# Kernel optimization log

Hardware: AMD Instinct MI355X
Metric: run time of the kernel (lower is better)

Reference implementation:

```python
import jax, jax.numpy as jnp
import numpy as np

MEM = 8192
FEAT = 512
B = 16
TAU_NEW = 0.85
D_MIN = 1.5
ALPHA = 0.5
EPS = 1e-8


def setup_inputs() -> dict:
    key = jax.random.key(0)
    k0, k1, k2, k3, k4, k5 = jax.random.split(key, 6)
    adj = (jax.random.uniform(k4, (MEM, MEM)) < 0.001).astype(jnp.float32)
    adj = jnp.maximum(adj, adj.T)  # symmetric, like the original writes
    return {
        "h_t": jax.random.normal(k0, (B, FEAT), jnp.float32),
        "current_position": jax.random.normal(k1, (B, 3), jnp.float32) * 3.0,
        "dones": jnp.zeros((B,), bool),
        "node_features": jax.random.normal(k2, (MEM, FEAT), jnp.float32),
        "node_positions": jax.random.normal(k3, (MEM, 3), jnp.float32) * 3.0,
        "adjacency_matrix": adj,
        "num_nodes": 4096,
        "ptr": 0,
        "last_visited_node_idx": jax.random.randint(k5, (B,), 0, 4096, jnp.int32),
    }


def reference(h_t, current_position, dones, node_features, node_positions,
              adjacency_matrix, num_nodes, ptr, last_visited_node_idx):
    M = node_features.shape[0]
    bsz = h_t.shape[0]
    idxs = jnp.arange(M)
    n0 = jnp.asarray(num_nodes, jnp.int32)
    p0 = jnp.asarray(ptr, jnp.int32)

    def step(state, xs):
        feat, pos, adj, p, n, lastv = state
        h_i, pos_i, done, i = xs
        # masked cosine-similarity search over active nodes (memory-bound matvec)
        fn = jnp.linalg.norm(feat, axis=-1)            # [M]
        hn = jnp.linalg.norm(h_i)
        sims = (feat @ h_i) / (jnp.maximum(fn, EPS) * jnp.maximum(hn, EPS))
        sims = jnp.where(idxs < n, sims, -2.0)
        best = jnp.argmax(sims).astype(jnp.int32)
        max_sim = sims[best]
        dist = jnp.linalg.norm(pos_i - pos[best])

        empty = n < 1
        should_add = (max_sim < TAU_NEW) | (dist > D_MIN)
        has_room = n < M
        # write index per branch: empty->0, add&room->n, add&full->ptr, else EMA at best
        widx = jnp.where(empty, 0,
                         jnp.where(should_add,
                                   jnp.where(has_room, n, p), best)).astype(jnp.int32)
        ema = (~empty) & (~should_add)
        new_f = jnp.where(ema, ALPHA * feat[widx] + (1.0 - ALPHA) * h_i, h_i)
        new_p = jnp.where(ema, ALPHA * pos[widx] + (1.0 - ALPHA) * pos_i, pos_i)
        # done -> no-op write
        new_f = jnp.where(done, feat[widx], new_f)
        new_p = jnp.where(done, pos[widx], new_p)
        feat = feat.at[widx].set(new_f)
        pos = pos.at[widx].set(new_p)
        n2 = n + jnp.where((~done) & (empty | (should_add & has_room)), 1, 0).astype(jnp.int32)
        p2 = jnp.where((~done) & (~empty) & should_add & (~has_room), (p + 1) % M, p)

        cur = widx
        last = lastv[i]
        do_edge = (~done) & (last != -1) & (last != cur)
        lc = jnp.clip(last, 0, M - 1)
        adj = adj.at[lc, cur].set(jnp.where(do_edge, 1.0, adj[lc, cur]))
        adj = adj.at[cur, lc].set(jnp.where(do_edge, 1.0, adj[cur, lc]))
        lastv = lastv.at[i].set(jnp.where(done, -1, cur))
        topo = jnp.where(done, 0.0, adj[cur].sum())
        return (feat, pos, adj, p2, n2, lastv), topo

    xs = (h_t, current_position, dones, jnp.arange(bsz, dtype=jnp.int32))
    state0 = (node_features, node_positions, adjacency_matrix, p0, n0,
              jnp.asarray(last_visited_node_idx, jnp.int32))
    _, topos = jax.lax.scan(step, state0, xs)
    return topos.reshape(bsz, 1)
```

## Files before the change

### kernel.cpp

```cpp
#include <hip/hip_runtime.h>
#include <cfloat>

#define MEMN 8192
#define FEATD 512
#define BATCH 16

static constexpr float TAU_NEW_C = 0.85f;
static constexpr float D_MIN_C  = 1.5f;
static constexpr float ALPHA_C  = 0.5f;
static constexpr float EPS_C    = 1e-8f;


__global__ __launch_bounds__(256) void score_pre_k(
    const float* __restrict__ h_t, const float* __restrict__ feat,
    const float* __restrict__ adj, const int* __restrict__ num_nodes,
    float* __restrict__ pv, int* __restrict__ pi,
    float* __restrict__ pre, float* __restrict__ hn, float* __restrict__ cross) {
  __shared__ float sh[BATCH * FEATD];
  __shared__ float red[256];
  __shared__ float sv[4][BATCH]; __shared__ int si[4][BATCH];
  const int b = blockIdx.x;
  const int tid = threadIdx.x;
  const int wave = tid >> 6, lane = tid & 63;

  if (b < 256) {
    for (int k = tid; k < BATCH * FEATD; k += 256) sh[k] = h_t[k];
    __syncthreads();
    const int n0 = *num_nodes;
    const int base = lane * 8;
    float best[BATCH]; int bidx[BATCH];
    #pragma unroll
    for (int i = 0; i < BATCH; ++i) { best[i] = -FLT_MAX; bidx[i] = 0x7fffffff; }
    for (int j = 0; j < 8; ++j) {
      const int row = b + ((j * 4 + wave) << 8);
      if (row >= n0) continue;
      const float4* fr = (const float4*)(feat + (size_t)row * FEATD);
      const float4 a0 = fr[lane * 2], a1 = fr[lane * 2 + 1];
      float sq = a0.x*a0.x + a0.y*a0.y + a0.z*a0.z + a0.w*a0.w
               + a1.x*a1.x + a1.y*a1.y + a1.z*a1.z + a1.w*a1.w;
      float acc[BATCH];
      #pragma unroll
      for (int i = 0; i < BATCH; ++i) {
        const float4 b0 = *(const float4*)(sh + i * FEATD + base);
        const float4 b1 = *(const float4*)(sh + i * FEATD + base + 4);
        acc[i] = a0.x*b0.x + a0.y*b0.y + a0.z*b0.z + a0.w*b0.w
               + a1.x*b1.x + a1.y*b1.y + a1.z*b1.z + a1.w*b1.w;
      }
      #pragma unroll
      for (int off = 32; off; off >>= 1) {
        sq += __shfl_down(sq, off);
        #pragma unroll
        for (int i = 0; i < BATCH; ++i) acc[i] += __shfl_down(acc[i], off);
      }
      if (lane == 0) {
        const float inv = 1.0f / fmaxf(sqrtf(sq), EPS_C);
        #pragma unroll
        for (int i = 0; i < BATCH; ++i) {
          const float v = acc[i] * inv;
          if (v > best[i]) { best[i] = v; bidx[i] = row; }
        }
      }
    }
    if (lane == 0) {
      #pragma unroll
      for (int i = 0; i < BATCH; ++i) { sv[wave][i] = best[i]; si[wave][i] = bidx[i]; }
    }
    __syncthreads();
    if (tid < BATCH) {
      float v = sv[0][tid]; int ix = si[0][tid];
      #pragma unroll
      for (int w = 1; w < 4; ++w)
        if (sv[w][tid] > v || (sv[w][tid] == v && si[w][tid] < ix)) { v = sv[w][tid]; ix = si[w][tid]; }
      pv[tid * 256 + b] = v; pi[tid * 256 + b] = ix;
    }
  } else if (b < 272) {
    const int bb = b - 256;
    const int n0 = *num_nodes;
    const int row = min(n0 + bb, MEMN - 1);
    const float4* r4 = (const float4*)(adj + (size_t)row * MEMN);
    float s = 0.f;
    for (int k = tid; k < MEMN / 4; k += 256) { const float4 v = r4[k]; s += v.x + v.y + v.z + v.w; }
    red[tid] = s;
    __syncthreads();
    for (int st = 128; st; st >>= 1) { if (tid < st) red[tid] += red[tid + st]; __syncthreads(); }
    if (tid == 0) pre[bb] = red[0];
    __syncthreads();
    const float* h = h_t + bb * FEATD;
    float sq = 0.f;
    for (int k = tid; k < FEATD; k += 256) { const float x = h[k]; sq += x * x; }
    red[tid] = sq;
    __syncthreads();
    for (int st = 128; st; st >>= 1) { if (tid < st) red[tid] += red[tid + st]; __syncthreads(); }
    if (tid == 0) hn[bb] = sqrtf(red[0]);
  } else {
    for (int k = tid; k < BATCH * FEATD; k += 256) sh[k] = h_t[k];
    __syncthreads();
    const int base = lane * 8;
    for (int jt = 0; jt < 4; ++jt) {
      const int j = jt * 4 + wave;
      const float4 a0 = *(const float4*)(sh + j * FEATD + base);
      const float4 a1 = *(const float4*)(sh + j * FEATD + base + 4);
      float sq = a0.x*a0.x + a0.y*a0.y + a0.z*a0.z + a0.w*a0.w
               + a1.x*a1.x + a1.y*a1.y + a1.z*a1.z + a1.w*a1.w;
      float acc[BATCH];
      #pragma unroll
      for (int i = 0; i < BATCH; ++i) {
        const float4 b0 = *(const float4*)(sh + i * FEATD + base);
        const float4 b1 = *(const float4*)(sh + i * FEATD + base + 4);
        acc[i] = a0.x*b0.x + a0.y*b0.y + a0.z*b0.z + a0.w*b0.w
               + a1.x*b1.x + a1.y*b1.y + a1.z*b1.z + a1.w*b1.w;
      }
      #pragma unroll
      for (int off = 32; off; off >>= 1) {
        sq += __shfl_down(sq, off);
        #pragma unroll
        for (int i = 0; i < BATCH; ++i) acc[i] += __shfl_down(acc[i], off);
      }
      if (lane == 0) {
        const float inv = 1.0f / fmaxf(sqrtf(sq), EPS_C);
        #pragma unroll
        for (int i = 0; i < BATCH; ++i) cross[i * 16 + j] = acc[i] * inv;
      }
    }
  }
}

__global__ __launch_bounds__(256) void val_fb_k(
    const float* __restrict__ h_t, const float* __restrict__ posin,
    const unsigned char* __restrict__ dones, const int* __restrict__ lastv,
    const float* __restrict__ feat, const float* __restrict__ posns,
    const float* __restrict__ adj, const int* __restrict__ num_nodes,
    const int* __restrict__ ptr_in, const float* __restrict__ pv,
    const int* __restrict__ pi, const float* __restrict__ pre,
    const float* __restrict__ hn, const float* __restrict__ cross,
    float* __restrict__ out) {
  const int tid = threadIdx.x;
  const int wave = tid >> 6, lane = tid & 63;
  __shared__ float wv[BATCH][4]; __shared__ int wi[BATCH][4];
  __shared__ float s_out[BATCH];
  __shared__ int s_valid;
  const int n0 = *num_nodes;

  float adjval = 1.f;
  int lastp = -1;
  if (tid < BATCH) {
    lastp = lastv[tid];
    if (lastp != -1) {
      const int lc = min(max(lastp, 0), MEMN - 1);
      const int row = min(n0 + tid, MEMN - 1);
      adjval = adj[(size_t)row * MEMN + lc];
    }
  }

  float v[BATCH]; int ix[BATCH];
  #pragma unroll
  for (int s = 0; s < BATCH; ++s) { v[s] = pv[s * 256 + tid]; ix[s] = pi[s * 256 + tid]; }
  #pragma unroll
  for (int s = 0; s < BATCH; ++s) {
    float bv = v[s]; int bi = ix[s];
    #pragma unroll
    for (int off = 32; off; off >>= 1) {
      const float v2 = __shfl_down(bv, off);
      const int   i2 = __shfl_down(bi, off);
      if (v2 > bv || (v2 == bv && i2 < bi)) { bv = v2; bi = i2; }
    }
    if (lane == 0) { wv[s][wave] = bv; wi[s][wave] = bi; }
  }
  __syncthreads();
  int ok = 1;
  if (tid < BATCH) {
    const int s = tid;
    float bv = wv[s][0]; int bi = wi[s][0];
    #pragma unroll
    for (int w = 1; w < 4; ++w)
      if (wv[s][w] > bv || (wv[s][w] == bv && wi[s][w] < bi)) { bv = wv[s][w]; bi = wi[s][w]; }
    for (int j = 0; j < s; ++j) {
      const float cv2 = cross[s * 16 + j];
      if (cv2 > bv) { bv = cv2; bi = n0 + j; }
    }
    if (bi == 0x7fffffff) ok = 0;
    else {
      const float max_sim = bv / fmaxf(hn[s], EPS_C);
      float px, py, pz;
      if (bi >= n0) { const float* pp = posin + (size_t)(bi - n0) * 3; px = pp[0]; py = pp[1]; pz = pp[2]; }
      else          { const float* pp = posns + (size_t)bi * 3;        px = pp[0]; py = pp[1]; pz = pp[2]; }
      const float dx = posin[s * 3 + 0] - px;
      const float dy = posin[s * 3 + 1] - py;
      const float dz = posin[s * 3 + 2] - pz;
      const float dist = sqrtf(dx * dx + dy * dy + dz * dz);
      const bool should_add = (max_sim < TAU_NEW_C) || (dist > D_MIN_C);
      ok = (!dones[s]) && should_add && (lastp == -1 || lastp < n0);
      float o = pre[s];
      if (lastp != -1 && lastp != n0 + s) { if (adjval == 0.f) o += 1.f; }
      s_out[s] = o;
    }
  }
  const unsigned long long m = __ballot(tid < BATCH ? ok : 1);
  if (tid == 0) s_valid = ((~m == 0ull) && (n0 >= 1) && (n0 + BATCH <= MEMN)) ? 1 : 0;
  __syncthreads();
  if (s_valid) { if (tid < BATCH) out[tid] = s_out[tid]; return; }

  __shared__ float mf[16][FEATD];
  __shared__ float mp[16][3];
  __shared__ int   midx[16];
  __shared__ float sh[FEATD];
  __shared__ float rv[256]; __shared__ int ri[256];
  __shared__ int   edges[64][2];
  __shared__ int   s_n, s_p, s_ec, s_mc;
  __shared__ int   s_done, s_widx, s_ema, s_src, s_dst, s_fb;
  __shared__ float s_delta, s_sum;
  if (tid == 0) { s_n = n0; s_p = *ptr_in; s_ec = 0; s_mc = 0; }
  __syncthreads();

  for (int step = 0; step < BATCH; ++step) {
    for (int k = tid; k < FEATD; k += 256) sh[k] = h_t[step * FEATD + k];
    __syncthreads();
    const int n_cur = s_n, mc = s_mc;

    float bv = -FLT_MAX; int bi = 0x7fffffff;
    for (int r = wave; r < n_cur; r += 4) {
      const float* src = feat + (size_t)r * FEATD;
      for (int k = 0; k < 16; ++k)
        if (k < mc && midx[k] == r) src = mf[k];
      float dot = 0.f, sq2 = 0.f;
      for (int e = lane; e < FEATD; e += 64) {
        const float a = src[e], b2 = sh[e];
        dot += a * b2; sq2 += a * a;
      }
      #pragma unroll
      for (int off = 32; off; off >>= 1) {
        dot += __shfl_down(dot, off);
        sq2 += __shfl_down(sq2, off);
      }
      if (lane == 0) {
        const float vv = dot / fmaxf(sqrtf(sq2), EPS_C);
        if (vv > bv) { bv = vv; bi = r; }
      }
    }
    if (lane == 0) { rv[wave] = bv; ri[wave] = bi; }
    __syncthreads();

    if (tid == 0) {
      float fbv = rv[0]; int fbi = ri[0];
      for (int w = 1; w < 4; ++w)
        if (rv[w] > fbv || (rv[w] == fbv && ri[w] < fbi)) { fbv = rv[w]; fbi = ri[w]; }
      const int n = s_n, p = s_p;
      int best; float max_sim;
      if (n < 1) { best = 0; max_sim = -2.0f; }
      else { best = fbi; max_sim = fbv / fmaxf(hn[step], EPS_C); }
      int bsrc = -1;
      for (int k = 0; k < s_mc; ++k) if (midx[k] == best) bsrc = k;
      float pbx, pby, pbz;
      if (bsrc >= 0) { pbx = mp[bsrc][0]; pby = mp[bsrc][1]; pbz = mp[bsrc][2]; }
      else { const float* pb = posns + (size_t)best * 3; pbx = pb[0]; pby = pb[1]; pbz = pb[2]; }
      const float dx = posin[step * 3 + 0] - pbx;
      const float dy = posin[step * 3 + 1] - pby;
      const float dz = posin[step * 3 + 2] - pbz;
      const float dist = sqrtf(dx * dx + dy * dy + dz * dz);
      const int done = dones[step] ? 1 : 0;
      const bool empty = (n < 1);
      const bool should_add = (max_sim < TAU_NEW_C) || (dist > D_MIN_C);
      const bool has_room = (n < MEMN);
      const int widx = empty ? 0 : (should_add ? (has_room ? n : p) : best);
      const bool ema = (!empty) && (!should_add);
      int srcs = -1;
      for (int k = 0; k < s_mc; ++k) if (midx[k] == widx) srcs = k;
      int dsts = srcs;
      if (!done) {
        if (srcs < 0) { dsts = s_mc; midx[dsts] = widx; s_mc = dsts + 1; }
        if (empty || (should_add && has_room)) s_n = n + 1;
        if ((!empty) && should_add && (!has_room)) s_p = (p + 1) % MEMN;
        const int last = lastv[step];
        if (last != -1 && last != widx) {
          const int lc = min(max(last, 0), MEMN - 1);
          const int ec = s_ec;
          edges[ec][0] = lc;   edges[ec][1] = widx;
          edges[ec + 1][0] = widx; edges[ec + 1][1] = lc;
          s_ec = ec + 2;
        }
      }
      s_done = done; s_widx = widx; s_ema = ema ? 1 : 0; s_src = srcs; s_dst = dsts;
      s_delta = 0.f;
      s_fb = 0;
      if (!done) {
        if (widx >= n0 && widx < n0 + BATCH) s_sum = pre[widx - n0];
        else s_fb = 1;
      }
    }
    __syncthreads();

    if (!s_done) {
      const int widx = s_widx;
      float* dstf = mf[s_dst];
      if (s_ema) {
        const float* srcf = (s_src >= 0) ? mf[s_src] : (feat + (size_t)widx * FEATD);
        for (int k = tid; k < FEATD; k += 256)
          dstf[k] = ALPHA_C * srcf[k] + (1.f - ALPHA_C) * sh[k];
      } else {
        for (int k = tid; k < FEATD; k += 256) dstf[k] = sh[k];
      }
      if (tid < 3) {
        const float sp = (s_src >= 0) ? mp[s_src][tid] : posns[(size_t)widx * 3 + tid];
        mp[s_dst][tid] = s_ema ? (ALPHA_C * sp + (1.f - ALPHA_C) * posin[step * 3 + tid])
                               : posin[step * 3 + tid];
      }
      if (tid < s_ec) {
        const int cur = widx;
        if (edges[tid][0] == cur) {
          const int c = edges[tid][1];
          bool dup = false;
          for (int e2 = 0; e2 < tid; ++e2)
            if (edges[e2][0] == cur && edges[e2][1] == c) dup = true;
          if (!dup && adj[(size_t)cur * MEMN + c] == 0.f) atomicAdd(&s_delta, 1.f);
        }
      }
    }
    __syncthreads();

    if (s_fb) {
      const float* row = adj + (size_t)s_widx * MEMN;
      float s = 0.f;
      for (int k = tid; k < MEMN; k += 256) s += row[k];
      rv[tid] = s;
      __syncthreads();
      for (int st = 128; st; st >>= 1) { if (tid < st) rv[tid] += rv[tid + st]; __syncthreads(); }
      if (tid == 0) s_sum = rv[0];
      __syncthreads();
    }
    if (tid == 0) out[step] = s_done ? 0.f : (s_sum + s_delta);
    __syncthreads();
  }
}

extern "C" void kernel_launch(void* const* d_in, const int* in_sizes, int n_in,
                              void* d_out, int out_size, void* d_ws, size_t ws_size,
                              hipStream_t stream) {
  const float*         h_t       = (const float*)d_in[0];
  const float*         cur_pos   = (const float*)d_in[1];
  const unsigned char* dones     = (const unsigned char*)d_in[2];
  const float*         node_feat = (const float*)d_in[3];
  const float*         node_pos  = (const float*)d_in[4];
  const float*         adj       = (const float*)d_in[5];
  const int*           num_nodes = (const int*)d_in[6];
  const int*           ptr_in    = (const int*)d_in[7];
  const int*           lastv     = (const int*)d_in[8];
  float* out = (float*)d_out;

  float* pv    = (float*)d_ws;
  int*   pi    = (int*)(pv + BATCH * 256);
  float* pre   = (float*)(pi + BATCH * 256);
  float* hn    = pre + BATCH;
  float* cross = hn + BATCH;

  score_pre_k<<<273, 256, 0, stream>>>(h_t, node_feat, adj, num_nodes, pv, pi, pre, hn, cross);
  val_fb_k<<<1, 256, 0, stream>>>(h_t, cur_pos, dones, lastv, node_feat, node_pos,
                                  adj, num_nodes, ptr_in, pv, pi, pre, hn, cross, out);
}
```

Before: 30.07 us.

## Fuse scoring and validation kernels with last-block atomic counter handoff

Merges the two kernels into one 256-block launch. The last block to finish, found through an atomicInc counter and thread fences, runs the validation and fallback path, which removes a kernel launch boundary. The query vectors now live in registers instead of shared memory, and the 16 dot-product reductions use a butterfly transpose so each lane ends up holding one query's sum, cutting the shuffle count. The adjacency row sums and the cross-similarity work are spread over the first 80 scoring blocks. The cost is much higher register pressure, and correctness relies on the counter wrapping back to zero on every call.

Result: slower. 43.22 us (+43.8%).

```diff
diff --git a/kernel.cpp b/kernel.cpp
--- a/kernel.cpp
+++ b/kernel.cpp
@@ -10,161 +10,168 @@
 static constexpr float ALPHA_C  = 0.5f;
 static constexpr float EPS_C    = 1e-8f;
 
-
-__global__ __launch_bounds__(256) void score_pre_k(
-    const float* __restrict__ h_t, const float* __restrict__ feat,
-    const float* __restrict__ adj, const int* __restrict__ num_nodes,
-    float* __restrict__ pv, int* __restrict__ pi,
-    float* __restrict__ pre, float* __restrict__ hn, float* __restrict__ cross) {
-  __shared__ float sh[BATCH * FEATD];
-  __shared__ float red[256];
-  __shared__ float sv[4][BATCH]; __shared__ int si[4][BATCH];
-  const int b = blockIdx.x;
-  const int tid = threadIdx.x;
-  const int wave = tid >> 6, lane = tid & 63;
-
-  if (b < 256) {
-    for (int k = tid; k < BATCH * FEATD; k += 256) sh[k] = h_t[k];
-    __syncthreads();
-    const int n0 = *num_nodes;
-    const int base = lane * 8;
-    float best[BATCH]; int bidx[BATCH];
-    #pragma unroll
-    for (int i = 0; i < BATCH; ++i) { best[i] = -FLT_MAX; bidx[i] = 0x7fffffff; }
-    for (int j = 0; j < 8; ++j) {
-      const int row = b + ((j * 4 + wave) << 8);
-      if (row >= n0) continue;
-      const float4* fr = (const float4*)(feat + (size_t)row * FEATD);
-      const float4 a0 = fr[lane * 2], a1 = fr[lane * 2 + 1];
-      float sq = a0.x*a0.x + a0.y*a0.y + a0.z*a0.z + a0.w*a0.w
-               + a1.x*a1.x + a1.y*a1.y + a1.z*a1.z + a1.w*a1.w;
-      float acc[BATCH];
-      #pragma unroll
-      for (int i = 0; i < BATCH; ++i) {
-        const float4 b0 = *(const float4*)(sh + i * FEATD + base);
-        const float4 b1 = *(const float4*)(sh + i * FEATD + base + 4);
-        acc[i] = a0.x*b0.x + a0.y*b0.y + a0.z*b0.z + a0.w*b0.w
-               + a1.x*b1.x + a1.y*b1.y + a1.z*b1.z + a1.w*b1.w;
-      }
-      #pragma unroll
-      for (int off = 32; off; off >>= 1) {
-        sq += __shfl_down(sq, off);
-        #pragma unroll
-        for (int i = 0; i < BATCH; ++i) acc[i] += __shfl_down(acc[i], off);
-      }
-      if (lane == 0) {
-        const float inv = 1.0f / fmaxf(sqrtf(sq), EPS_C);
-        #pragma unroll
-        for (int i = 0; i < BATCH; ++i) {
-          const float v = acc[i] * inv;
-          if (v > best[i]) { best[i] = v; bidx[i] = row; }
-        }
-      }
-    }
-    if (lane == 0) {
-      #pragma unroll
-      for (int i = 0; i < BATCH; ++i) { sv[wave][i] = best[i]; si[wave][i] = bidx[i]; }
-    }
-    __syncthreads();
-    if (tid < BATCH) {
-      float v = sv[0][tid]; int ix = si[0][tid];
-      #pragma unroll
-      for (int w = 1; w < 4; ++w)
-        if (sv[w][tid] > v || (sv[w][tid] == v && si[w][tid] < ix)) { v = sv[w][tid]; ix = si[w][tid]; }
-      pv[tid * 256 + b] = v; pi[tid * 256 + b] = ix;
-    }
-  } else if (b < 272) {
-    const int bb = b - 256;
-    const int n0 = *num_nodes;
-    const int row = min(n0 + bb, MEMN - 1);
-    const float4* r4 = (const float4*)(adj + (size_t)row * MEMN);
-    float s = 0.f;
-    for (int k = tid; k < MEMN / 4; k += 256) { const float4 v = r4[k]; s += v.x + v.y + v.z + v.w; }
-    red[tid] = s;
-    __syncthreads();
-    for (int st = 128; st; st >>= 1) { if (tid < st) red[tid] += red[tid + st]; __syncthreads(); }
-    if (tid == 0) pre[bb] = red[0];
-    __syncthreads();
-    const float* h = h_t + bb * FEATD;
-    float sq = 0.f;
-    for (int k = tid; k < FEATD; k += 256) { const float x = h[k]; sq += x * x; }
-    red[tid] = sq;
-    __syncthreads();
-    for (int st = 128; st; st >>= 1) { if (tid < st) red[tid] += red[tid + st]; __syncthreads(); }
-    if (tid == 0) hn[bb] = sqrtf(red[0]);
-  } else {
-    for (int k = tid; k < BATCH * FEATD; k += 256) sh[k] = h_t[k];
-    __syncthreads();
-    const int base = lane * 8;
-    for (int jt = 0; jt < 4; ++jt) {
-      const int j = jt * 4 + wave;
-      const float4 a0 = *(const float4*)(sh + j * FEATD + base);
-      const float4 a1 = *(const float4*)(sh + j * FEATD + base + 4);
-      float sq = a0.x*a0.x + a0.y*a0.y + a0.z*a0.z + a0.w*a0.w
-               + a1.x*a1.x + a1.y*a1.y + a1.z*a1.z + a1.w*a1.w;
-      float acc[BATCH];
-      #pragma unroll
-      for (int i = 0; i < BATCH; ++i) {
-        const float4 b0 = *(const float4*)(sh + i * FEATD + base);
-        const float4 b1 = *(const float4*)(sh + i * FEATD + base + 4);
-        acc[i] = a0.x*b0.x + a0.y*b0.y + a0.z*b0.z + a0.w*b0.w
-               + a1.x*b1.x + a1.y*b1.y + a1.z*b1.z + a1.w*b1.w;
-      }
-      #pragma unroll
-      for (int off = 32; off; off >>= 1) {
-        sq += __shfl_down(sq, off);
-        #pragma unroll
-        for (int i = 0; i < BATCH; ++i) acc[i] += __shfl_down(acc[i], off);
-      }
-      if (lane == 0) {
-        const float inv = 1.0f / fmaxf(sqrtf(sq), EPS_C);
-        #pragma unroll
-        for (int i = 0; i < BATCH; ++i) cross[i * 16 + j] = acc[i] * inv;
-      }
-    }
-  }
-}
-
-__global__ __launch_bounds__(256) void val_fb_k(
+__device__ __forceinline__ int brev4(int l) {
+  return ((l & 1) << 3) | ((l & 2) << 1) | ((l & 4) >> 1) | ((l & 8) >> 3);
+}
+__device__ __forceinline__ float dot8(const float4& a0, const float4& a1,
+                                      const float4& b0, const float4& b1) {
+  return a0.x*b0.x + a0.y*b0.y + a0.z*b0.z + a0.w*b0.w
+       + a1.x*b1.x + a1.y*b1.y + a1.z*b1.z + a1.w*b1.w;
+}
+
+__device__ __forceinline__ float tree_reduce16(float acc[BATCH], int lane) {
+  #pragma unroll
+  for (int k = 0; k < 8; ++k) {
+    const bool hi = (lane & 1);
+    const float mine = hi ? acc[k + 8] : acc[k];
+    const float send = hi ? acc[k] : acc[k + 8];
+    acc[k] = mine + __shfl_xor(send, 1);
+  }
+  #pragma unroll
+  for (int k = 0; k < 4; ++k) {
+    const bool hi = (lane & 2);
+    const float mine = hi ? acc[k + 4] : acc[k];
+    const float send = hi ? acc[k] : acc[k + 4];
+    acc[k] = mine + __shfl_xor(send, 2);
+  }
+  #pragma unroll
+  for (int k = 0; k < 2; ++k) {
+    const bool hi = (lane & 4);
+    const float mine = hi ? acc[k + 2] : acc[k];
+    const float send = hi ? acc[k] : acc[k + 2];
+    acc[k] = mine + __shfl_xor(send, 4);
+  }
+  {
+    const bool hi = (lane & 8);
+    const float mine = hi ? acc[1] : acc[0];
+    const float send = hi ? acc[0] : acc[1];
+    acc[0] = mine + __shfl_xor(send, 8);
+  }
+  acc[0] += __shfl_xor(acc[0], 16);
+  acc[0] += __shfl_xor(acc[0], 32);
+  return acc[0];
+}
+
+__global__ __launch_bounds__(256, 1) void fused_k(
     const float* __restrict__ h_t, const float* __restrict__ posin,
     const unsigned char* __restrict__ dones, const int* __restrict__ lastv,
     const float* __restrict__ feat, const float* __restrict__ posns,
     const float* __restrict__ adj, const int* __restrict__ num_nodes,
-    const int* __restrict__ ptr_in, const float* __restrict__ pv,
-    const int* __restrict__ pi, const float* __restrict__ pre,
-    const float* __restrict__ hn, const float* __restrict__ cross,
-    float* __restrict__ out) {
+    const int* __restrict__ ptr_in,
+    float* __restrict__ pv, int* __restrict__ pi, float* __restrict__ pre4,
+    float* __restrict__ hnw, float* __restrict__ cross,
+    unsigned* counter, float* __restrict__ out)
+{
+  const int b = blockIdx.x;
   const int tid = threadIdx.x;
   const int wave = tid >> 6, lane = tid & 63;
-  __shared__ float wv[BATCH][4]; __shared__ int wi[BATCH][4];
-  __shared__ float s_out[BATCH];
-  __shared__ int s_valid;
   const int n0 = *num_nodes;
 
-  float adjval = 1.f;
-  int lastp = -1;
+  __shared__ float sv[4][BATCH]; __shared__ int si[4][BATCH];
+  __shared__ float red4[4];
+  __shared__ int s_last;
+
+  float adjval = 1.f; int lastp = -1;
   if (tid < BATCH) {
     lastp = lastv[tid];
     if (lastp != -1) {
       const int lc = min(max(lastp, 0), MEMN - 1);
-      const int row = min(n0 + tid, MEMN - 1);
-      adjval = adj[(size_t)row * MEMN + lc];
-    }
-  }
-
-  float v[BATCH]; int ix[BATCH];
+      adjval = adj[(size_t)min(n0 + tid, MEMN - 1) * MEMN + lc];
+    }
+  }
+
+  float4 hA[BATCH], hB[BATCH];
   #pragma unroll
-  for (int s = 0; s < BATCH; ++s) { v[s] = pv[s * 256 + tid]; ix[s] = pi[s * 256 + tid]; }
-  #pragma unroll
-  for (int s = 0; s < BATCH; ++s) {
-    float bv = v[s]; int bi = ix[s];
-    #pragma unroll
-    for (int off = 32; off; off >>= 1) {
-      const float v2 = __shfl_down(bv, off);
-      const int   i2 = __shfl_down(bi, off);
-      if (v2 > bv || (v2 == bv && i2 < bi)) { bv = v2; bi = i2; }
-    }
-    if (lane == 0) { wv[s][wave] = bv; wi[s][wave] = bi; }
+  for (int i = 0; i < BATCH; ++i) {
+    const float4* hp = (const float4*)(h_t + i * FEATD + lane * 8);
+    hA[i] = hp[0]; hB[i] = hp[1];
+  }
+
+  float bestv = -FLT_MAX; int besti = 0x7fffffff;
+  for (int j = 0; j < 8; ++j) {
+    const int row = b + ((j * 4 + wave) << 8);
+    if (row >= n0) break;
+    const float4* fr = (const float4*)(feat + (size_t)row * FEATD + lane * 8);
+    const float4 a0 = fr[0], a1 = fr[1];
+    float acc[BATCH];
+    #pragma unroll
+    for (int i = 0; i < BATCH; ++i) acc[i] = dot8(a0, a1, hA[i], hB[i]);
+    float sq = dot8(a0, a1, a0, a1);
+    #pragma unroll
+    for (int m = 1; m <= 32; m <<= 1) sq += __shfl_xor(sq, m);
+    const float dtot = tree_reduce16(acc, lane);
+    const float v = dtot / fmaxf(sqrtf(sq), EPS_C);
+    if (v > bestv) { bestv = v; besti = row; }
+  }
+  if (lane < BATCH) { sv[wave][brev4(lane)] = bestv; si[wave][brev4(lane)] = besti; }
+  __syncthreads();
+  if (tid < BATCH) {
+    float v = sv[0][tid]; int ix = si[0][tid];
+    #pragma unroll
+    for (int w = 1; w < 4; ++w)
+      if (sv[w][tid] > v || (sv[w][tid] == v && si[w][tid] < ix)) { v = sv[w][tid]; ix = si[w][tid]; }
+    pv[tid * 256 + b] = v; pi[tid * 256 + b] = ix;
+  }
+
+  if (b < 64) {
+    const int row = min(n0 + (b >> 2), MEMN - 1);
+    const float4* r4 = (const float4*)(adj + (size_t)row * MEMN + (size_t)(b & 3) * 2048);
+    const float4 q0 = r4[tid], q1 = r4[tid + 256];
+    float s = q0.x+q0.y+q0.z+q0.w + q1.x+q1.y+q1.z+q1.w;
+    #pragma unroll
+    for (int m = 1; m <= 32; m <<= 1) s += __shfl_xor(s, m);
+    if (lane == 0) red4[wave] = s;
+    __syncthreads();
+    if (tid == 0) pre4[b] = red4[0] + red4[1] + red4[2] + red4[3];
+  } else if (b < 80) {
+    const int j = b - 64;
+    if (wave == 0) {
+      float4 c0 = hA[0], c1 = hB[0];
+      #pragma unroll
+      for (int jj = 1; jj < BATCH; ++jj) if (j == jj) { c0 = hA[jj]; c1 = hB[jj]; }
+      float acc[BATCH];
+      #pragma unroll
+      for (int i = 0; i < BATCH; ++i) acc[i] = dot8(c0, c1, hA[i], hB[i]);
+      const float d = tree_reduce16(acc, lane);
+      const float djj = __shfl(d, brev4(j));
+      const float inv = 1.f / fmaxf(sqrtf(djj), EPS_C);
+      if (lane == 0) hnw[j] = sqrtf(djj);
+      if (lane < BATCH) cross[brev4(lane) * 16 + j] = d * inv;
+    }
+  }
+
+  __threadfence();
+  __syncthreads();
+  if (tid == 0) {
+    const unsigned old = atomicInc(counter, 255u);
+    s_last = (old == 254u) ? 1 : 0;
+  }
+  __syncthreads();
+  if (!s_last) return;
+  __threadfence();
+
+  __shared__ float wv[BATCH][4]; __shared__ int wi[BATCH][4];
+  __shared__ float preS[BATCH]; __shared__ float s_outv[BATCH];
+  __shared__ int s_valid;
+
+  if (tid < BATCH)
+    preS[tid] = pre4[tid*4+0] + pre4[tid*4+1] + pre4[tid*4+2] + pre4[tid*4+3];
+
+  {
+    float vv2[BATCH]; int ii2[BATCH];
+    #pragma unroll
+    for (int s = 0; s < BATCH; ++s) { vv2[s] = pv[s * 256 + tid]; ii2[s] = pi[s * 256 + tid]; }
+    #pragma unroll
+    for (int s = 0; s < BATCH; ++s) {
+      float bv = vv2[s]; int bi = ii2[s];
+      #pragma unroll
+      for (int off = 32; off; off >>= 1) {
+        const float v2 = __shfl_down(bv, off);
+        const int   i2 = __shfl_down(bi, off);
+        if (v2 > bv || (v2 == bv && i2 < bi)) { bv = v2; bi = i2; }
+      }
+      if (lane == 0) { wv[s][wave] = bv; wi[s][wave] = bi; }
+    }
   }
   __syncthreads();
   int ok = 1;
@@ -180,7 +187,7 @@
     }
     if (bi == 0x7fffffff) ok = 0;
     else {
-      const float max_sim = bv / fmaxf(hn[s], EPS_C);
+      const float max_sim = bv / fmaxf(hnw[s], EPS_C);
       float px, py, pz;
       if (bi >= n0) { const float* pp = posin + (size_t)(bi - n0) * 3; px = pp[0]; py = pp[1]; pz = pp[2]; }
       else          { const float* pp = posns + (size_t)bi * 3;        px = pp[0]; py = pp[1]; pz = pp[2]; }
@@ -190,21 +197,21 @@
       const float dist = sqrtf(dx * dx + dy * dy + dz * dz);
       const bool should_add = (max_sim < TAU_NEW_C) || (dist > D_MIN_C);
       ok = (!dones[s]) && should_add && (lastp == -1 || lastp < n0);
-      float o = pre[s];
+      float o = preS[s];
       if (lastp != -1 && lastp != n0 + s) { if (adjval == 0.f) o += 1.f; }
-      s_out[s] = o;
-    }
-  }
-  const unsigned long long m = __ballot(tid < BATCH ? ok : 1);
-  if (tid == 0) s_valid = ((~m == 0ull) && (n0 >= 1) && (n0 + BATCH <= MEMN)) ? 1 : 0;
-  __syncthreads();
-  if (s_valid) { if (tid < BATCH) out[tid] = s_out[tid]; return; }
+      s_outv[s] = o;
+    }
+  }
+  const unsigned long long mball = __ballot(tid < BATCH ? ok : 1);
+  if (tid == 0) s_valid = ((~mball == 0ull) && (n0 >= 1) && (n0 + BATCH <= MEMN)) ? 1 : 0;
+  __syncthreads();
+  if (s_valid) { if (tid < BATCH) out[tid] = s_outv[tid]; return; }
 
   __shared__ float mf[16][FEATD];
   __shared__ float mp[16][3];
   __shared__ int   midx[16];
-  __shared__ float sh[FEATD];
-  __shared__ float rv[256]; __shared__ int ri[256];
+  __shared__ float shF[FEATD];
+  __shared__ float rvF[256]; __shared__ int riF[256];
   __shared__ int   edges[64][2];
   __shared__ int   s_n, s_p, s_ec, s_mc;
   __shared__ int   s_done, s_widx, s_ema, s_src, s_dst, s_fb;
@@ -213,7 +220,7 @@
   __syncthreads();
 
   for (int step = 0; step < BATCH; ++step) {
-    for (int k = tid; k < FEATD; k += 256) sh[k] = h_t[step * FEATD + k];
+    for (int k = tid; k < FEATD; k += 256) shF[k] = h_t[step * FEATD + k];
     __syncthreads();
     const int n_cur = s_n, mc = s_mc;
 
@@ -224,7 +231,7 @@
         if (k < mc && midx[k] == r) src = mf[k];
       float dot = 0.f, sq2 = 0.f;
       for (int e = lane; e < FEATD; e += 64) {
-        const float a = src[e], b2 = sh[e];
+        const float a = src[e], b2 = shF[e];
         dot += a * b2; sq2 += a * a;
       }
       #pragma unroll
@@ -237,17 +244,17 @@
         if (vv > bv) { bv = vv; bi = r; }
       }
     }
-    if (lane == 0) { rv[wave] = bv; ri[wave] = bi; }
+    if (lane == 0) { rvF[wave] = bv; riF[wave] = bi; }
     __syncthreads();
 
     if (tid == 0) {
-      float fbv = rv[0]; int fbi = ri[0];
+      float fbv = rvF[0]; int fbi = riF[0];
       for (int w = 1; w < 4; ++w)
-        if (rv[w] > fbv || (rv[w] == fbv && ri[w] < fbi)) { fbv = rv[w]; fbi = ri[w]; }
+        if (rvF[w] > fbv || (rvF[w] == fbv && riF[w] < fbi)) { fbv = rvF[w]; fbi = riF[w]; }
       const int n = s_n, p = s_p;
       int best; float max_sim;
       if (n < 1) { best = 0; max_sim = -2.0f; }
-      else { best = fbi; max_sim = fbv / fmaxf(hn[step], EPS_C); }
+      else { best = fbi; max_sim = fbv / fmaxf(hnw[step], EPS_C); }
       int bsrc = -1;
       for (int k = 0; k < s_mc; ++k) if (midx[k] == best) bsrc = k;
       float pbx, pby, pbz;
@@ -283,7 +290,7 @@
       s_delta = 0.f;
       s_fb = 0;
       if (!done) {
-        if (widx >= n0 && widx < n0 + BATCH) s_sum = pre[widx - n0];
+        if (widx >= n0 && widx < n0 + BATCH) s_sum = preS[widx - n0];
         else s_fb = 1;
       }
     }
@@ -295,9 +302,9 @@
       if (s_ema) {
         const float* srcf = (s_src >= 0) ? mf[s_src] : (feat + (size_t)widx * FEATD);
         for (int k = tid; k < FEATD; k += 256)
-          dstf[k] = ALPHA_C * srcf[k] + (1.f - ALPHA_C) * sh[k];
+          dstf[k] = ALPHA_C * srcf[k] + (1.f - ALPHA_C) * shF[k];
       } else {
-        for (int k = tid; k < FEATD; k += 256) dstf[k] = sh[k];
+        for (int k = tid; k < FEATD; k += 256) dstf[k] = shF[k];
       }
       if (tid < 3) {
         const float sp = (s_src >= 0) ? mp[s_src][tid] : posns[(size_t)widx * 3 + tid];
@@ -318,13 +325,13 @@
     __syncthreads();
 
     if (s_fb) {
-      const float* row = adj + (size_t)s_widx * MEMN;
+      const float* rowp = adj + (size_t)s_widx * MEMN;
       float s = 0.f;
-      for (int k = tid; k < MEMN; k += 256) s += row[k];
-      rv[tid] = s;
+      for (int k = tid; k < MEMN; k += 256) s += rowp[k];
+      rvF[tid] = s;
       __syncthreads();
-      for (int st = 128; st; st >>= 1) { if (tid < st) rv[tid] += rv[tid + st]; __syncthreads(); }
-      if (tid == 0) s_sum = rv[0];
+      for (int st = 128; st; st >>= 1) { if (tid < st) rvF[tid] += rvF[tid + st]; __syncthreads(); }
+      if (tid == 0) s_sum = rvF[0];
       __syncthreads();
     }
     if (tid == 0) out[step] = s_done ? 0.f : (s_sum + s_delta);
@@ -346,13 +353,14 @@
   const int*           lastv     = (const int*)d_in[8];
   float* out = (float*)d_out;
 
-  float* pv    = (float*)d_ws;
-  int*   pi    = (int*)(pv + BATCH * 256);
-  float* pre   = (float*)(pi + BATCH * 256);
-  float* hn    = pre + BATCH;
-  float* cross = hn + BATCH;
-
-  score_pre_k<<<273, 256, 0, stream>>>(h_t, node_feat, adj, num_nodes, pv, pi, pre, hn, cross);
-  val_fb_k<<<1, 256, 0, stream>>>(h_t, cur_pos, dones, lastv, node_feat, node_pos,
-                                  adj, num_nodes, ptr_in, pv, pi, pre, hn, cross, out);
-}
+  float*    pv      = (float*)d_ws;
+  int*      pi      = (int*)(pv + BATCH * 256);
+  float*    pre4    = (float*)(pi + BATCH * 256);
+  float*    hnw     = pre4 + 64;
+  float*    cross   = hnw + BATCH;
+  unsigned* counter = (unsigned*)(cross + 256);
+
+  fused_k<<<256, 256, 0, stream>>>(h_t, cur_pos, dones, lastv, node_feat, node_pos,
+                                   adj, num_nodes, ptr_in,
+                                   pv, pi, pre4, hnw, cross, counter, out);
+}
```
